# Optimization experiments

Measured on AMD Instinct MI355X. Metric: run time of the kernel, lower is better.

## Reference

```python
import jax, jax.numpy as jnp
import numpy as np

LAMBDA = 0.7
K = 3
HIDDEN = 8
IN_F = 512
OUT_F = 256
N = 4096


def _gat_layer(x, adj, W, a):
    # h = fc(x); e[i,j] = attn([h_i ; h_j]) = h_i @ a[:F] + h_j @ a[F:]
    # (same math as the N*N repeat/cat/linear, without materializing [N*N, 2F])
    h = x @ W                      # [N, F]
    F_ = h.shape[1]
    src = h @ a[:F_]               # [N, 1]
    dst = h @ a[F_:]               # [N, 1]
    e = src + dst.T                # [N, N]
    att = jax.nn.softmax(e, axis=1) * adj
    return jax.nn.elu(att @ h)     # [N, F]


def setup_inputs() -> dict:
    key = jax.random.key(0)
    ks = jax.random.split(key, 8)
    x = jax.random.normal(ks[0], (N, IN_F), dtype=jnp.float32)
    # binarized sparse-ish adjacency stored densely (avg degree ~41)
    adj = (jax.random.uniform(ks[1], (N, N)) < 0.01).astype(jnp.float32)
    W1 = jax.random.normal(ks[2], (IN_F, HIDDEN), dtype=jnp.float32) * (1.0 / np.sqrt(IN_F))
    a1 = jax.random.normal(ks[3], (2 * HIDDEN, 1), dtype=jnp.float32) * (1.0 / np.sqrt(2 * HIDDEN))
    W2 = jax.random.normal(ks[4], (HIDDEN, 1), dtype=jnp.float32) * (1.0 / np.sqrt(HIDDEN))
    a2 = jax.random.normal(ks[5], (2, 1), dtype=jnp.float32)
    W_sgc = jax.random.normal(ks[6], (IN_F * K, OUT_F), dtype=jnp.float32) * (1.0 / np.sqrt(IN_F * K))
    b_sgc = jnp.zeros((OUT_F,), dtype=jnp.float32)
    return {"x": x, "adj": adj, "W1": W1, "a1": a1, "W2": W2, "a2": a2,
            "W_sgc": W_sgc, "b_sgc": b_sgc}


def reference(x, adj, W1, a1, W2, a2, W_sgc, b_sgc):
    # GAT scoring head (dropout p=0.6 is identity at inference)
    h1 = _gat_layer(x, adj, W1, a1)
    node_scores = _gat_layer(h1, adj, W2, a2)        # [N, 1]

    # K-hop adjacency powers
    adj_list = [adj]
    for _ in range(1, K):
        adj_list.append(adj_list[-1] @ adj)

    # dynamic per-row masking (row-broadcast of node_scores > lambda)
    change_mask = (node_scores > LAMBDA).astype(adj.dtype)  # [N, 1] broadcasts over cols
    for k in range(K - 1):
        adj_list[k] = adj_list[k] * change_mask
        adj_list[k + 1] = adj_list[k + 1] * (1.0 - change_mask)

    # SGC: concat K hop-aggregated features, then linear
    agg = jnp.concatenate([A @ x for A in adj_list], axis=1)  # [N, K*IN_F]
    return agg @ W_sgc + b_sgc
```

## Files before the change

kernel.cpp:

```cpp
#include <hip/hip_runtime.h>
#include <hip/hip_bf16.h>
#include <cstddef>

#define NNODE 4096
#define INF   512
#define OUTF  256
#define HID   8
#define CAP   128

typedef __attribute__((ext_vector_type(8))) short short8;
typedef __attribute__((ext_vector_type(4))) float f32x4;

__device__ __forceinline__ unsigned short f2bf(float f){
  unsigned int u = __float_as_uint(f);
  u += 0x7fffu + ((u >> 16) & 1u);
  return (unsigned short)(u >> 16);
}

__global__ __launch_bounds__(256) void build_csr(const float* __restrict__ adj,
                                                 int* __restrict__ deg,
                                                 int* __restrict__ cols){
  int row = blockIdx.x, tid = threadIdx.x;
  __shared__ int cnt;
  if (tid == 0) cnt = 0;
  __syncthreads();
  const float4* arow = (const float4*)(adj + (size_t)row * NNODE);
  int* crow = cols + (size_t)row * CAP;
  #pragma unroll
  for (int k = 0; k < 4; k++){
    int idx = k * 256 + tid;
    float4 v = arow[idx];
    int n0 = (v.x != 0.f), n1 = (v.y != 0.f), n2 = (v.z != 0.f), n3 = (v.w != 0.f);
    int m = n0 + n1 + n2 + n3;
    if (m){
      int base = atomicAdd(&cnt, m);
      int c = idx * 4;
      if (n0){ if (base < CAP) crow[base] = c;     base++; }
      if (n1){ if (base < CAP) crow[base] = c + 1; base++; }
      if (n2){ if (base < CAP) crow[base] = c + 2; base++; }
      if (n3){ if (base < CAP) crow[base] = c + 3; }
    }
  }
  __syncthreads();
  if (tid == 0) deg[row] = cnt > CAP ? CAP : cnt;
}

__global__ __launch_bounds__(256) void gat_h(const float* __restrict__ x,
                                             const float* __restrict__ W1,
                                             const float* __restrict__ a1,
                                             float* __restrict__ h,
                                             float* __restrict__ dstv,
                                             unsigned short* __restrict__ xb){
  int wave = threadIdx.x >> 6, lane = threadIdx.x & 63;
  int row = blockIdx.x * 4 + wave;
  const float* xr = x + (size_t)row * INF;
  unsigned short* xbr = xb + (size_t)row * INF;
  float acc[HID];
  #pragma unroll
  for (int f = 0; f < HID; f++) acc[f] = 0.f;
  for (int k = lane; k < INF; k += 64){
    float xv = xr[k];
    xbr[k] = f2bf(xv);
    const float* wp = W1 + (size_t)k * HID;
    #pragma unroll
    for (int f = 0; f < HID; f++) acc[f] += xv * wp[f];
  }
  #pragma unroll
  for (int f = 0; f < HID; f++)
    for (int o = 32; o >= 1; o >>= 1) acc[f] += __shfl_xor(acc[f], o, 64);
  if (lane == 0){
    float d = 0.f;
    #pragma unroll
    for (int f = 0; f < HID; f++){ h[(size_t)row*HID + f] = acc[f]; d += acc[f] * a1[HID + f]; }
    dstv[row] = d;
  }
}

__global__ __launch_bounds__(256) void gat_agg1_f(const float* __restrict__ h,
                                                  const float* __restrict__ dstv,
                                                  const int* __restrict__ deg,
                                                  const int* __restrict__ cols,
                                                  const float* __restrict__ W2,
                                                  float* __restrict__ h2){
  __shared__ float p[NNODE];
  __shared__ float red[4];
  int tid = threadIdx.x, lane = tid & 63, wv = tid >> 6;
  float mx = -INFINITY;
  for (int i = tid; i < NNODE; i += 256) mx = fmaxf(mx, dstv[i]);
  #pragma unroll
  for (int o = 32; o >= 1; o >>= 1) mx = fmaxf(mx, __shfl_xor(mx, o, 64));
  if (lane == 0) red[wv] = mx;
  __syncthreads();
  mx = fmaxf(fmaxf(red[0], red[1]), fmaxf(red[2], red[3]));
  __syncthreads();
  float sum = 0.f;
  for (int i = tid; i < NNODE; i += 256){ float e = expf(dstv[i] - mx); p[i] = e; sum += e; }
  #pragma unroll
  for (int o = 32; o >= 1; o >>= 1) sum += __shfl_xor(sum, o, 64);
  if (lane == 0) red[wv] = sum;
  __syncthreads();
  float inv = 1.0f / (red[0] + red[1] + red[2] + red[3]);
  for (int i = tid; i < NNODE; i += 256) p[i] *= inv;
  __syncthreads();

  int f = tid & 7, rg = tid >> 3;
  int row = blockIdx.x * 32 + rg;
  const int* cl = cols + (size_t)row * CAP;
  int d = deg[row];
  float acc = 0.f;
  for (int n = 0; n < d; n++){
    int j = cl[n];
    acc += p[j] * h[(size_t)j * HID + f];
  }
  float e = acc > 0.f ? acc : expm1f(acc);
  float t = e * W2[f];
  t += __shfl_xor(t, 1, 64);
  t += __shfl_xor(t, 2, 64);
  t += __shfl_xor(t, 4, 64);
  if (f == 0) h2[row] = t;
}

__global__ __launch_bounds__(256) void scores_mask_f(const float* __restrict__ h2,
                                                     const float* __restrict__ a2,
                                                     const int* __restrict__ deg,
                                                     const int* __restrict__ cols,
                                                     float* __restrict__ maskf){
  __shared__ float q[NNODE];
  __shared__ float red[4];
  int tid = threadIdx.x, lane = tid & 63, wv = tid >> 6;
  float s2 = a2[1];
  float mx = -INFINITY;
  for (int i = tid; i < NNODE; i += 256) mx = fmaxf(mx, s2 * h2[i]);
  #pragma unroll
  for (int o = 32; o >= 1; o >>= 1) mx = fmaxf(mx, __shfl_xor(mx, o, 64));
  if (lane == 0) red[wv] = mx;
  __syncthreads();
  mx = fmaxf(fmaxf(red[0], red[1]), fmaxf(red[2], red[3]));
  __syncthreads();
  float sum = 0.f;
  for (int i = tid; i < NNODE; i += 256){ float e = expf(s2 * h2[i] - mx); q[i] = e; sum += e; }
  #pragma unroll
  for (int o = 32; o >= 1; o >>= 1) sum += __shfl_xor(sum, o, 64);
  if (lane == 0) red[wv] = sum;
  __syncthreads();
  float inv = 1.0f / (red[0] + red[1] + red[2] + red[3]);
  for (int i = tid; i < NNODE; i += 256) q[i] = q[i] * inv * h2[i];
  __syncthreads();

  int row = blockIdx.x * 256 + tid;
  const int* cl = cols + (size_t)row * CAP;
  int d = deg[row];
  float s = 0.f;
  for (int n = 0; n < d; n++) s += q[cl[n]];
  float e = s > 0.f ? s : expm1f(s);
  maskf[row] = (e > 0.7f) ? 1.0f : 0.0f;
}

__global__ void convert_w(const float* __restrict__ Wsgc, unsigned short* __restrict__ wbT){
  int idx = blockIdx.x * 256 + threadIdx.x;
  if (idx >= 512 * 512) return;
  int c = idx >> 9, k = idx & 511;
  float val = (c < 256) ? Wsgc[(size_t)k * OUTF + c]
                        : Wsgc[(size_t)(1024 + k) * OUTF + (c - 256)];
  wbT[idx] = f2bf(val);
}

__global__ __launch_bounds__(256) void gemm_xw(const unsigned short* __restrict__ XB,
                                               const unsigned short* __restrict__ BT,
                                               float* __restrict__ G){
  __shared__ unsigned short As[128][72];
  __shared__ unsigned short Bs[128][72];
  int tid = threadIdx.x;
  int wave = tid >> 6, lane = tid & 63;
  int row0 = blockIdx.x * 128;
  int col0 = blockIdx.y * 128;
  int wr = wave >> 1, wc = wave & 1;
  f32x4 acc[4][4];
  #pragma unroll
  for (int i = 0; i < 4; i++)
    #pragma unroll
    for (int j = 0; j < 4; j++)
      #pragma unroll
      for (int e = 0; e < 4; e++) acc[i][j][e] = 0.f;

  int mrow = lane & 15;
  int kq = (lane >> 4) * 8;

  for (int k0 = 0; k0 < 512; k0 += 64){
    #pragma unroll
    for (int ps = 0; ps < 4; ps++){
      int idx = ps * 256 + tid;
      int r = idx >> 3;
      int ko = (idx & 7) * 8;
      *(int4*)(&As[r][ko]) = *(const int4*)(XB + ((size_t)(row0 + r) * 512 + k0 + ko));
      *(int4*)(&Bs[r][ko]) = *(const int4*)(BT + ((size_t)(col0 + r) * 512 + k0 + ko));
    }
    __syncthreads();
    #pragma unroll
    for (int kk = 0; kk < 2; kk++){
      short8 a[4], b[4];
      #pragma unroll
      for (int i = 0; i < 4; i++)
        a[i] = *(const short8*)(&As[wr * 64 + i * 16 + mrow][kk * 32 + kq]);
      #pragma unroll
      for (int j = 0; j < 4; j++)
        b[j] = *(const short8*)(&Bs[wc * 64 + j * 16 + mrow][kk * 32 + kq]);
      #pragma unroll
      for (int i = 0; i < 4; i++)
        #pragma unroll
        for (int j = 0; j < 4; j++)
          acc[i][j] = __builtin_amdgcn_mfma_f32_16x16x32_bf16(a[i], b[j], acc[i][j], 0, 0, 0);
    }
    __syncthreads();
  }
  int crow = (lane >> 4) * 4;
  int ccol = lane & 15;
  #pragma unroll
  for (int i = 0; i < 4; i++)
    #pragma unroll
    for (int j = 0; j < 4; j++)
      #pragma unroll
      for (int e = 0; e < 4; e++){
        int r = row0 + wr * 64 + i * 16 + crow + e;
        int c = col0 + wc * 64 + j * 16 + ccol;
        G[(size_t)r * 512 + c] = acc[i][j][e];
      }
}

__global__ __launch_bounds__(256) void hop4(const float* __restrict__ in, int instride,
                                            float* __restrict__ out,
                                            const int* __restrict__ deg,
                                            const int* __restrict__ cols){
  int wave = threadIdx.x >> 6, lane = threadIdx.x & 63;
  int row = blockIdx.x * 4 + wave;
  const int* cl = cols + (size_t)row * CAP;
  int d = deg[row];
  f32x4 acc = {0.f, 0.f, 0.f, 0.f};
  f32x4 acc2 = {0.f, 0.f, 0.f, 0.f};
  int n = 0;
  for (; n + 8 <= d; n += 8){
    int j0 = cl[n],   j1 = cl[n+1], j2 = cl[n+2], j3 = cl[n+3];
    int j4 = cl[n+4], j5 = cl[n+5], j6 = cl[n+6], j7 = cl[n+7];
    f32x4 a = ((const f32x4*)(in + (size_t)j0 * instride))[lane];
    f32x4 b = ((const f32x4*)(in + (size_t)j1 * instride))[lane];
    f32x4 c = ((const f32x4*)(in + (size_t)j2 * instride))[lane];
    f32x4 e = ((const f32x4*)(in + (size_t)j3 * instride))[lane];
    f32x4 f = ((const f32x4*)(in + (size_t)j4 * instride))[lane];
    f32x4 g = ((const f32x4*)(in + (size_t)j5 * instride))[lane];
    f32x4 hh = ((const f32x4*)(in + (size_t)j6 * instride))[lane];
    f32x4 ii = ((const f32x4*)(in + (size_t)j7 * instride))[lane];
    acc  += a + b + c + e;
    acc2 += f + g + hh + ii;
  }
  for (; n + 4 <= d; n += 4){
    int j0 = cl[n], j1 = cl[n+1], j2 = cl[n+2], j3 = cl[n+3];
    f32x4 a = ((const f32x4*)(in + (size_t)j0 * instride))[lane];
    f32x4 b = ((const f32x4*)(in + (size_t)j1 * instride))[lane];
    f32x4 c = ((const f32x4*)(in + (size_t)j2 * instride))[lane];
    f32x4 e = ((const f32x4*)(in + (size_t)j3 * instride))[lane];
    acc += a + b + c + e;
  }
  for (; n < d; n++)
    acc += ((const f32x4*)(in + (size_t)cl[n] * instride))[lane];
  ((f32x4*)(out + (size_t)row * OUTF))[lane] = acc + acc2;
}

__global__ __launch_bounds__(256) void hop_final(const float* __restrict__ Gleft,
                                                 const float* __restrict__ T2,
                                                 const float* __restrict__ maskf,
                                                 const float* __restrict__ b,
                                                 float* __restrict__ out,
                                                 const int* __restrict__ deg,
                                                 const int* __restrict__ cols){
  int wave = threadIdx.x >> 6, lane = threadIdx.x & 63;
  int row = blockIdx.x * 4 + wave;
  const int* cl = cols + (size_t)row * CAP;
  int d = deg[row];
  bool m = maskf[row] != 0.0f;
  const float* in = m ? Gleft : T2;
  int instride    = m ? 512   : 256;
  f32x4 acc = {0.f, 0.f, 0.f, 0.f};
  f32x4 acc2 = {0.f, 0.f, 0.f, 0.f};
  int n = 0;
  for (; n + 8 <= d; n += 8){
    int j0 = cl[n],   j1 = cl[n+1], j2 = cl[n+2], j3 = cl[n+3];
    int j4 = cl[n+4], j5 = cl[n+5], j6 = cl[n+6], j7 = cl[n+7];
    f32x4 a = ((const f32x4*)(in + (size_t)j0 * instride))[lane];
    f32x4 bb = ((const f32x4*)(in + (size_t)j1 * instride))[lane];
    f32x4 c = ((const f32x4*)(in + (size_t)j2 * instride))[lane];
    f32x4 e = ((const f32x4*)(in + (size_t)j3 * instride))[lane];
    f32x4 f = ((const f32x4*)(in + (size_t)j4 * instride))[lane];
    f32x4 g = ((const f32x4*)(in + (size_t)j5 * instride))[lane];
    f32x4 hh = ((const f32x4*)(in + (size_t)j6 * instride))[lane];
    f32x4 ii = ((const f32x4*)(in + (size_t)j7 * instride))[lane];
    acc  += a + bb + c + e;
    acc2 += f + g + hh + ii;
  }
  for (; n + 4 <= d; n += 4){
    int j0 = cl[n], j1 = cl[n+1], j2 = cl[n+2], j3 = cl[n+3];
    f32x4 a = ((const f32x4*)(in + (size_t)j0 * instride))[lane];
    f32x4 bb = ((const f32x4*)(in + (size_t)j1 * instride))[lane];
    f32x4 c = ((const f32x4*)(in + (size_t)j2 * instride))[lane];
    f32x4 e = ((const f32x4*)(in + (size_t)j3 * instride))[lane];
    acc += a + bb + c + e;
  }
  for (; n < d; n++)
    acc += ((const f32x4*)(in + (size_t)cl[n] * instride))[lane];
  f32x4 bias = ((const f32x4*)b)[lane];
  ((f32x4*)(out + (size_t)row * OUTF))[lane] = acc + acc2 + bias;
}

extern "C" void kernel_launch(void* const* d_in, const int* in_sizes, int n_in,
                              void* d_out, int out_size, void* d_ws, size_t ws_size,
                              hipStream_t stream) {
  const float* x    = (const float*)d_in[0];
  const float* adj  = (const float*)d_in[1];
  const float* W1   = (const float*)d_in[2];
  const float* a1   = (const float*)d_in[3];
  const float* W2   = (const float*)d_in[4];
  const float* a2   = (const float*)d_in[5];
  const float* Wsgc = (const float*)d_in[6];
  const float* bsgc = (const float*)d_in[7];
  float* out = (float*)d_out;

  char* w = (char*)d_ws;
  size_t off = 0;
  auto carve = [&](size_t bytes) -> char* {
    char* p = w + off;
    off += (bytes + 255) & ~(size_t)255;
    return p;
  };
  int*   deg   = (int*)carve((size_t)NNODE * 4);
  int*   cols  = (int*)carve((size_t)NNODE * CAP * 4);
  float* h     = (float*)carve((size_t)NNODE * HID * 4);
  float* dstv  = (float*)carve((size_t)NNODE * 4);
  float* h2    = (float*)carve((size_t)NNODE * 4);
  float* maskf = (float*)carve((size_t)NNODE * 4);
  unsigned short* wbT = (unsigned short*)carve((size_t)512 * 512 * 2);
  unsigned short* xb  = (unsigned short*)carve((size_t)NNODE * INF * 2);
  float* G  = (float*)carve((size_t)NNODE * 512 * 4);
  float* T1 = (float*)carve((size_t)NNODE * OUTF * 4);
  float* T2 = (float*)carve((size_t)NNODE * OUTF * 4);

  build_csr<<<NNODE, 256, 0, stream>>>(adj, deg, cols);

  gat_h<<<NNODE / 4, 256, 0, stream>>>(x, W1, a1, h, dstv, xb);
  gat_agg1_f<<<NNODE / 32, 256, 0, stream>>>(h, dstv, deg, cols, W2, h2);
  scores_mask_f<<<NNODE / 256, 256, 0, stream>>>(h2, a2, deg, cols, maskf);

  convert_w<<<1024, 256, 0, stream>>>(Wsgc, wbT);
  dim3 gg(32, 4);
  gemm_xw<<<gg, 256, 0, stream>>>(xb, wbT, G);

  hop4<<<NNODE / 4, 256, 0, stream>>>(G + 256, 512, T1, deg, cols);
  hop4<<<NNODE / 4, 256, 0, stream>>>(T1, 256, T2, deg, cols);
  hop_final<<<NNODE / 4, 256, 0, stream>>>(G, T2, maskf, bsgc, out, deg, cols);
}
```

Before: 188.7 us.

## Split softmax into single-block kernels, widen GAT aggregation, shrink GEMM tiles, halve hop columns

The softmax normalisation is moved out of the per-block GAT kernels into dedicated single-block 1024-thread kernels, so each aggregation block no longer recomputes the full 4096-element softmax. The aggregation and mask kernels now use a wave per row with lanes splitting neighbours. The GEMM tile drops from 128x128 to 64x64 to launch more blocks. Each hop kernel is split into two column-half launches with f32x2 loads. This adds four more kernel launches and serial single-block phases, and the hop split doubles index reads.

After: 205.6 us. +9.0%, slower.

```diff
diff --git a/kernel.cpp b/kernel.cpp
--- a/kernel.cpp
+++ b/kernel.cpp
@@ -10,6 +10,7 @@
 
 typedef __attribute__((ext_vector_type(8))) short short8;
 typedef __attribute__((ext_vector_type(4))) float f32x4;
+typedef __attribute__((ext_vector_type(2))) float f32x2;
 
 __device__ __forceinline__ unsigned short f2bf(float f){
   unsigned int u = __float_as_uint(f);
@@ -76,84 +77,106 @@
   }
 }
 
-__global__ __launch_bounds__(256) void gat_agg1_f(const float* __restrict__ h,
-                                                  const float* __restrict__ dstv,
-                                                  const int* __restrict__ deg,
-                                                  const int* __restrict__ cols,
-                                                  const float* __restrict__ W2,
-                                                  float* __restrict__ h2){
-  __shared__ float p[NNODE];
-  __shared__ float red[4];
+__global__ __launch_bounds__(1024) void softmax_p(const float* __restrict__ dstv,
+                                                  float* __restrict__ p){
+  __shared__ float red[16];
   int tid = threadIdx.x, lane = tid & 63, wv = tid >> 6;
   float mx = -INFINITY;
-  for (int i = tid; i < NNODE; i += 256) mx = fmaxf(mx, dstv[i]);
+  for (int i = tid; i < NNODE; i += 1024) mx = fmaxf(mx, dstv[i]);
   #pragma unroll
   for (int o = 32; o >= 1; o >>= 1) mx = fmaxf(mx, __shfl_xor(mx, o, 64));
   if (lane == 0) red[wv] = mx;
   __syncthreads();
-  mx = fmaxf(fmaxf(red[0], red[1]), fmaxf(red[2], red[3]));
+  mx = red[0];
+  #pragma unroll
+  for (int k = 1; k < 16; k++) mx = fmaxf(mx, red[k]);
   __syncthreads();
   float sum = 0.f;
-  for (int i = tid; i < NNODE; i += 256){ float e = expf(dstv[i] - mx); p[i] = e; sum += e; }
+  for (int i = tid; i < NNODE; i += 1024){ float e = expf(dstv[i] - mx); p[i] = e; sum += e; }
   #pragma unroll
   for (int o = 32; o >= 1; o >>= 1) sum += __shfl_xor(sum, o, 64);
   if (lane == 0) red[wv] = sum;
   __syncthreads();
-  float inv = 1.0f / (red[0] + red[1] + red[2] + red[3]);
-  for (int i = tid; i < NNODE; i += 256) p[i] *= inv;
-  __syncthreads();
-
-  int f = tid & 7, rg = tid >> 3;
-  int row = blockIdx.x * 32 + rg;
+  float tot = 0.f;
+  #pragma unroll
+  for (int k = 0; k < 16; k++) tot += red[k];
+  float inv = 1.0f / tot;
+  for (int i = tid; i < NNODE; i += 1024) p[i] *= inv;
+}
+
+__global__ __launch_bounds__(256) void gat_agg1(const float* __restrict__ h,
+                                                const float* __restrict__ p,
+                                                const int* __restrict__ deg,
+                                                const int* __restrict__ cols,
+                                                const float* __restrict__ W2,
+                                                float* __restrict__ h2){
+  int wave = threadIdx.x >> 6, lane = threadIdx.x & 63;
+  int row = blockIdx.x * 4 + wave;
   const int* cl = cols + (size_t)row * CAP;
   int d = deg[row];
+  int ng = lane >> 3;
+  int f  = lane & 7;
   float acc = 0.f;
-  for (int n = 0; n < d; n++){
+  for (int n = ng; n < d; n += 8){
     int j = cl[n];
     acc += p[j] * h[(size_t)j * HID + f];
   }
+  acc += __shfl_xor(acc, 8, 64);
+  acc += __shfl_xor(acc, 16, 64);
+  acc += __shfl_xor(acc, 32, 64);
   float e = acc > 0.f ? acc : expm1f(acc);
   float t = e * W2[f];
   t += __shfl_xor(t, 1, 64);
   t += __shfl_xor(t, 2, 64);
   t += __shfl_xor(t, 4, 64);
-  if (f == 0) h2[row] = t;
-}
-
-__global__ __launch_bounds__(256) void scores_mask_f(const float* __restrict__ h2,
-                                                     const float* __restrict__ a2,
-                                                     const int* __restrict__ deg,
-                                                     const int* __restrict__ cols,
-                                                     float* __restrict__ maskf){
-  __shared__ float q[NNODE];
-  __shared__ float red[4];
+  if (lane == 0) h2[row] = t;
+}
+
+__global__ __launch_bounds__(1024) void softmax_q(const float* __restrict__ h2,
+                                                  const float* __restrict__ a2,
+                                                  float* __restrict__ q){
+  __shared__ float red[16];
   int tid = threadIdx.x, lane = tid & 63, wv = tid >> 6;
   float s2 = a2[1];
   float mx = -INFINITY;
-  for (int i = tid; i < NNODE; i += 256) mx = fmaxf(mx, s2 * h2[i]);
+  for (int i = tid; i < NNODE; i += 1024) mx = fmaxf(mx, s2 * h2[i]);
   #pragma unroll
   for (int o = 32; o >= 1; o >>= 1) mx = fmaxf(mx, __shfl_xor(mx, o, 64));
   if (lane == 0) red[wv] = mx;
   __syncthreads();
-  mx = fmaxf(fmaxf(red[0], red[1]), fmaxf(red[2], red[3]));
+  mx = red[0];
+  #pragma unroll
+  for (int k = 1; k < 16; k++) mx = fmaxf(mx, red[k]);
   __syncthreads();
   float sum = 0.f;
-  for (int i = tid; i < NNODE; i += 256){ float e = expf(s2 * h2[i] - mx); q[i] = e; sum += e; }
+  for (int i = tid; i < NNODE; i += 1024){ float e = expf(s2 * h2[i] - mx); q[i] = e; sum += e; }
   #pragma unroll
   for (int o = 32; o >= 1; o >>= 1) sum += __shfl_xor(sum, o, 64);
   if (lane == 0) red[wv] = sum;
   __syncthreads();
-  float inv = 1.0f / (red[0] + red[1] + red[2] + red[3]);
-  for (int i = tid; i < NNODE; i += 256) q[i] = q[i] * inv * h2[i];
-  __syncthreads();
-
-  int row = blockIdx.x * 256 + tid;
+  float tot = 0.f;
+  #pragma unroll
+  for (int k = 0; k < 16; k++) tot += red[k];
+  float inv = 1.0f / tot;
+  for (int i = tid; i < NNODE; i += 1024) q[i] = q[i] * inv * h2[i];
+}
+
+__global__ __launch_bounds__(256) void scores_mask(const float* __restrict__ q,
+                                                   const int* __restrict__ deg,
+                                                   const int* __restrict__ cols,
+                                                   float* __restrict__ maskf){
+  int wave = threadIdx.x >> 6, lane = threadIdx.x & 63;
+  int row = blockIdx.x * 4 + wave;
   const int* cl = cols + (size_t)row * CAP;
   int d = deg[row];
   float s = 0.f;
-  for (int n = 0; n < d; n++) s += q[cl[n]];
-  float e = s > 0.f ? s : expm1f(s);
-  maskf[row] = (e > 0.7f) ? 1.0f : 0.0f;
+  for (int n = lane; n < d; n += 64) s += q[cl[n]];
+  #pragma unroll
+  for (int o = 32; o >= 1; o >>= 1) s += __shfl_xor(s, o, 64);
+  if (lane == 0){
+    float e = s > 0.f ? s : expm1f(s);
+    maskf[row] = (e > 0.7f) ? 1.0f : 0.0f;
+  }
 }
 
 __global__ void convert_w(const float* __restrict__ Wsgc, unsigned short* __restrict__ wbT){
@@ -168,18 +191,18 @@
 __global__ __launch_bounds__(256) void gemm_xw(const unsigned short* __restrict__ XB,
                                                const unsigned short* __restrict__ BT,
                                                float* __restrict__ G){
-  __shared__ unsigned short As[128][72];
-  __shared__ unsigned short Bs[128][72];
+  __shared__ unsigned short As[64][72];
+  __shared__ unsigned short Bs[64][72];
   int tid = threadIdx.x;
   int wave = tid >> 6, lane = tid & 63;
-  int row0 = blockIdx.x * 128;
-  int col0 = blockIdx.y * 128;
+  int row0 = blockIdx.x * 64;
+  int col0 = blockIdx.y * 64;
   int wr = wave >> 1, wc = wave & 1;
-  f32x4 acc[4][4];
-  #pragma unroll
-  for (int i = 0; i < 4; i++)
-    #pragma unroll
-    for (int j = 0; j < 4; j++)
+  f32x4 acc[2][2];
+  #pragma unroll
+  for (int i = 0; i < 2; i++)
+    #pragma unroll
+    for (int j = 0; j < 2; j++)
       #pragma unroll
       for (int e = 0; e < 4; e++) acc[i][j][e] = 0.f;
 
@@ -188,7 +211,7 @@
 
   for (int k0 = 0; k0 < 512; k0 += 64){
     #pragma unroll
-    for (int ps = 0; ps < 4; ps++){
+    for (int ps = 0; ps < 2; ps++){
       int idx = ps * 256 + tid;
       int r = idx >> 3;
       int ko = (idx & 7) * 8;
@@ -198,17 +221,17 @@
     __syncthreads();
     #pragma unroll
     for (int kk = 0; kk < 2; kk++){
-      short8 a[4], b[4];
-      #pragma unroll
-      for (int i = 0; i < 4; i++)
-        a[i] = *(const short8*)(&As[wr * 64 + i * 16 + mrow][kk * 32 + kq]);
-      #pragma unroll
-      for (int j = 0; j < 4; j++)
-        b[j] = *(const short8*)(&Bs[wc * 64 + j * 16 + mrow][kk * 32 + kq]);
-      #pragma unroll
-      for (int i = 0; i < 4; i++)
+      short8 a[2], b[2];
+      #pragma unroll
+      for (int i = 0; i < 2; i++)
+        a[i] = *(const short8*)(&As[wr * 32 + i * 16 + mrow][kk * 32 + kq]);
+      #pragma unroll
+      for (int j = 0; j < 2; j++)
+        b[j] = *(const short8*)(&Bs[wc * 32 + j * 16 + mrow][kk * 32 + kq]);
+      #pragma unroll
+      for (int i = 0; i < 2; i++)
         #pragma unroll
-        for (int j = 0; j < 4; j++)
+        for (int j = 0; j < 2; j++)
           acc[i][j] = __builtin_amdgcn_mfma_f32_16x16x32_bf16(a[i], b[j], acc[i][j], 0, 0, 0);
     }
     __syncthreads();
@@ -216,98 +239,85 @@
   int crow = (lane >> 4) * 4;
   int ccol = lane & 15;
   #pragma unroll
-  for (int i = 0; i < 4; i++)
-    #pragma unroll
-    for (int j = 0; j < 4; j++)
+  for (int i = 0; i < 2; i++)
+    #pragma unroll
+    for (int j = 0; j < 2; j++)
       #pragma unroll
       for (int e = 0; e < 4; e++){
-        int r = row0 + wr * 64 + i * 16 + crow + e;
-        int c = col0 + wc * 64 + j * 16 + ccol;
+        int r = row0 + wr * 32 + i * 16 + crow + e;
+        int c = col0 + wc * 32 + j * 16 + ccol;
         G[(size_t)r * 512 + c] = acc[i][j][e];
       }
 }
 
-__global__ __launch_bounds__(256) void hop4(const float* __restrict__ in, int instride,
-                                            float* __restrict__ out,
-                                            const int* __restrict__ deg,
-                                            const int* __restrict__ cols){
+__global__ __launch_bounds__(256) void hop_half(const float* __restrict__ in, int instride,
+                                                int colbase,
+                                                float* __restrict__ out,
+                                                const int* __restrict__ deg,
+                                                const int* __restrict__ cols){
   int wave = threadIdx.x >> 6, lane = threadIdx.x & 63;
   int row = blockIdx.x * 4 + wave;
   const int* cl = cols + (size_t)row * CAP;
   int d = deg[row];
-  f32x4 acc = {0.f, 0.f, 0.f, 0.f};
-  f32x4 acc2 = {0.f, 0.f, 0.f, 0.f};
+  const float* src = in + colbase;
+  f32x2 acc = {0.f, 0.f};
+  f32x2 acc2 = {0.f, 0.f};
   int n = 0;
   for (; n + 8 <= d; n += 8){
     int j0 = cl[n],   j1 = cl[n+1], j2 = cl[n+2], j3 = cl[n+3];
     int j4 = cl[n+4], j5 = cl[n+5], j6 = cl[n+6], j7 = cl[n+7];
-    f32x4 a = ((const f32x4*)(in + (size_t)j0 * instride))[lane];
-    f32x4 b = ((const f32x4*)(in + (size_t)j1 * instride))[lane];
-    f32x4 c = ((const f32x4*)(in + (size_t)j2 * instride))[lane];
-    f32x4 e = ((const f32x4*)(in + (size_t)j3 * instride))[lane];
-    f32x4 f = ((const f32x4*)(in + (size_t)j4 * instride))[lane];
-    f32x4 g = ((const f32x4*)(in + (size_t)j5 * instride))[lane];
-    f32x4 hh = ((const f32x4*)(in + (size_t)j6 * instride))[lane];
-    f32x4 ii = ((const f32x4*)(in + (size_t)j7 * instride))[lane];
+    f32x2 a = ((const f32x2*)(src + (size_t)j0 * instride))[lane];
+    f32x2 b = ((const f32x2*)(src + (size_t)j1 * instride))[lane];
+    f32x2 c = ((const f32x2*)(src + (size_t)j2 * instride))[lane];
+    f32x2 e = ((const f32x2*)(src + (size_t)j3 * instride))[lane];
+    f32x2 f = ((const f32x2*)(src + (size_t)j4 * instride))[lane];
+    f32x2 g = ((const f32x2*)(src + (size_t)j5 * instride))[lane];
+    f32x2 hh = ((const f32x2*)(src + (size_t)j6 * instride))[lane];
+    f32x2 ii = ((const f32x2*)(src + (size_t)j7 * instride))[lane];
     acc  += a + b + c + e;
     acc2 += f + g + hh + ii;
   }
-  for (; n + 4 <= d; n += 4){
-    int j0 = cl[n], j1 = cl[n+1], j2 = cl[n+2], j3 = cl[n+3];
-    f32x4 a = ((const f32x4*)(in + (size_t)j0 * instride))[lane];
-    f32x4 b = ((const f32x4*)(in + (size_t)j1 * instride))[lane];
-    f32x4 c = ((const f32x4*)(in + (size_t)j2 * instride))[lane];
-    f32x4 e = ((const f32x4*)(in + (size_t)j3 * instride))[lane];
-    acc += a + b + c + e;
-  }
   for (; n < d; n++)
-    acc += ((const f32x4*)(in + (size_t)cl[n] * instride))[lane];
-  ((f32x4*)(out + (size_t)row * OUTF))[lane] = acc + acc2;
-}
-
-__global__ __launch_bounds__(256) void hop_final(const float* __restrict__ Gleft,
-                                                 const float* __restrict__ T2,
-                                                 const float* __restrict__ maskf,
-                                                 const float* __restrict__ b,
-                                                 float* __restrict__ out,
-                                                 const int* __restrict__ deg,
-                                                 const int* __restrict__ cols){
+    acc += ((const f32x2*)(src + (size_t)cl[n] * instride))[lane];
+  ((f32x2*)(out + (size_t)row * OUTF + colbase))[lane] = acc + acc2;
+}
+
+__global__ __launch_bounds__(256) void hop_final_half(const float* __restrict__ Gleft,
+                                                      const float* __restrict__ T2,
+                                                      const float* __restrict__ maskf,
+                                                      const float* __restrict__ b,
+                                                      int colbase,
+                                                      float* __restrict__ out,
+                                                      const int* __restrict__ deg,
+                                                      const int* __restrict__ cols){
   int wave = threadIdx.x >> 6, lane = threadIdx.x & 63;
   int row = blockIdx.x * 4 + wave;
   const int* cl = cols + (size_t)row * CAP;
   int d = deg[row];
   bool m = maskf[row] != 0.0f;
-  const float* in = m ? Gleft : T2;
+  const float* src = (m ? Gleft : T2) + colbase;
   int instride    = m ? 512   : 256;
-  f32x4 acc = {0.f, 0.f, 0.f, 0.f};
-  f32x4 acc2 = {0.f, 0.f, 0.f, 0.f};
+  f32x2 acc = {0.f, 0.f};
+  f32x2 acc2 = {0.f, 0.f};
   int n = 0;
   for (; n + 8 <= d; n += 8){
     int j0 = cl[n],   j1 = cl[n+1], j2 = cl[n+2], j3 = cl[n+3];
     int j4 = cl[n+4], j5 = cl[n+5], j6 = cl[n+6], j7 = cl[n+7];
-    f32x4 a = ((const f32x4*)(in + (size_t)j0 * instride))[lane];
-    f32x4 bb = ((const f32x4*)(in + (size_t)j1 * instride))[lane];
-    f32x4 c = ((const f32x4*)(in + (size_t)j2 * instride))[lane];
-    f32x4 e = ((const f32x4*)(in + (size_t)j3 * instride))[lane];
-    f32x4 f = ((const f32x4*)(in + (size_t)j4 * instride))[lane];
-    f32x4 g = ((const f32x4*)(in + (size_t)j5 * instride))[lane];
-    f32x4 hh = ((const f32x4*)(in + (size_t)j6 * instride))[lane];
-    f32x4 ii = ((const f32x4*)(in + (size_t)j7 * instride))[lane];
+    f32x2 a = ((const f32x2*)(src + (size_t)j0 * instride))[lane];
+    f32x2 bb = ((const f32x2*)(src + (size_t)j1 * instride))[lane];
+    f32x2 c = ((const f32x2*)(src + (size_t)j2 * instride))[lane];
+    f32x2 e = ((const f32x2*)(src + (size_t)j3 * instride))[lane];
+    f32x2 f = ((const f32x2*)(src + (size_t)j4 * instride))[lane];
+    f32x2 g = ((const f32x2*)(src + (size_t)j5 * instride))[lane];
+    f32x2 hh = ((const f32x2*)(src + (size_t)j6 * instride))[lane];
+    f32x2 ii = ((const f32x2*)(src + (size_t)j7 * instride))[lane];
     acc  += a + bb + c + e;
     acc2 += f + g + hh + ii;
   }
-  for (; n + 4 <= d; n += 4){
-    int j0 = cl[n], j1 = cl[n+1], j2 = cl[n+2], j3 = cl[n+3];
-    f32x4 a = ((const f32x4*)(in + (size_t)j0 * instride))[lane];
-    f32x4 bb = ((const f32x4*)(in + (size_t)j1 * instride))[lane];
-    f32x4 c = ((const f32x4*)(in + (size_t)j2 * instride))[lane];
-    f32x4 e = ((const f32x4*)(in + (size_t)j3 * instride))[lane];
-    acc += a + bb + c + e;
-  }
   for (; n < d; n++)
-    acc += ((const f32x4*)(in + (size_t)cl[n] * instride))[lane];
-  f32x4 bias = ((const f32x4*)b)[lane];
-  ((f32x4*)(out + (size_t)row * OUTF))[lane] = acc + acc2 + bias;
+    acc += ((const f32x2*)(src + (size_t)cl[n] * instride))[lane];
+  f32x2 bias = ((const f32x2*)(b + colbase))[lane];
+  ((f32x2*)(out + (size_t)row * OUTF + colbase))[lane] = acc + acc2 + bias;
 }
 
 extern "C" void kernel_launch(void* const* d_in, const int* in_sizes, int n_in,
@@ -334,7 +344,9 @@
   int*   cols  = (int*)carve((size_t)NNODE * CAP * 4);
   float* h     = (float*)carve((size_t)NNODE * HID * 4);
   float* dstv  = (float*)carve((size_t)NNODE * 4);
+  float* p     = (float*)carve((size_t)NNODE * 4);
   float* h2    = (float*)carve((size_t)NNODE * 4);
+  float* q     = (float*)carve((size_t)NNODE * 4);
   float* maskf = (float*)carve((size_t)NNODE * 4);
   unsigned short* wbT = (unsigned short*)carve((size_t)512 * 512 * 2);
   unsigned short* xb  = (unsigned short*)carve((size_t)NNODE * INF * 2);
@@ -345,14 +357,19 @@
   build_csr<<<NNODE, 256, 0, stream>>>(adj, deg, cols);
 
   gat_h<<<NNODE / 4, 256, 0, stream>>>(x, W1, a1, h, dstv, xb);
-  gat_agg1_f<<<NNODE / 32, 256, 0, stream>>>(h, dstv, deg, cols, W2, h2);
-  scores_mask_f<<<NNODE / 256, 256, 0, stream>>>(h2, a2, deg, cols, maskf);
+  softmax_p<<<1, 1024, 0, stream>>>(dstv, p);
+  gat_agg1<<<NNODE / 4, 256, 0, stream>>>(h, p, deg, cols, W2, h2);
+  softmax_q<<<1, 1024, 0, stream>>>(h2, a2, q);
+  scores_mask<<<NNODE / 4, 256, 0, stream>>>(q, deg, cols, maskf);
 
   convert_w<<<1024, 256, 0, stream>>>(Wsgc, wbT);
-  dim3 gg(32, 4);
+  dim3 gg(64, 8);
   gemm_xw<<<gg, 256, 0, stream>>>(xb, wbT, G);
 
-  hop4<<<NNODE / 4, 256, 0, stream>>>(G + 256, 512, T1, deg, cols);
-  hop4<<<NNODE / 4, 256, 0, stream>>>(T1, 256, T2, deg, cols);
-  hop_final<<<NNODE / 4, 256, 0, stream>>>(G, T2, maskf, bsgc, out, deg, cols);
-}
+  hop_half<<<NNODE / 4, 256, 0, stream>>>(G + 256, 512, 0,   T1, deg, cols);
+  hop_half<<<NNODE / 4, 256, 0, stream>>>(G + 256, 512, 128, T1, deg, cols);
+  hop_half<<<NNODE / 4, 256, 0, stream>>>(T1, 256, 0,   T2, deg, cols);
+  hop_half<<<NNODE / 4, 256, 0, stream>>>(T1, 256, 128, T2, deg, cols);
+  hop_final_half<<<NNODE / 4, 256, 0, stream>>>(G, T2, maskf, bsgc, 0,   out, deg, cols);
+  hop_final_half<<<NNODE / 4, 256, 0, stream>>>(G, T2, maskf, bsgc, 128, out, deg, cols);
+}
```
